# Performance work log

Measured on AMD Instinct MI355X. Metric: run time of the kernel, lower is better.

Reference implementation:

```python
import jax, jax.numpy as jnp
import numpy as np


def _dwconv3x3(x, w, b):
    # depthwise 3x3, stride 1, padding 1 (groups == channels)
    y = jax.lax.conv_general_dilated(
        x, w, window_strides=(1, 1), padding=((1, 1), (1, 1)),
        dimension_numbers=('NCHW', 'OIHW', 'NCHW'),
        feature_group_count=x.shape[1])
    return y + b[None, :, None, None]


def _maxpool(x, f):
    # adaptive_max_pool2d to (h//f, w//f) with h,w divisible by f == stride-f max pool
    return jax.lax.reduce_window(x, -jnp.inf, jax.lax.max,
                                 (1, 1, f, f), (1, 1, f, f), 'VALID')


def _up_nearest(x, f):
    return jnp.repeat(jnp.repeat(x, f, axis=2), f, axis=3)


def setup_inputs() -> dict:
    key = jax.random.key(0)
    ks = jax.random.split(key, 10)
    B, C, H, W = 4, 32, 128, 128
    x = jax.random.normal(ks[0], (B, C, H, W), dtype=jnp.float32)
    mk = lambda k, shape, s: jax.random.normal(k, shape, dtype=jnp.float32) * s
    return {
        'x': x,
        'w0': mk(ks[1], (C, 1, 3, 3), 0.3), 'b0': mk(ks[2], (C,), 0.05),
        'w1': mk(ks[3], (C, 1, 3, 3), 0.3), 'b1': mk(ks[4], (C,), 0.05),
        'w2': mk(ks[5], (C, 1, 3, 3), 0.3), 'b2': mk(ks[6], (C,), 0.05),
        'wa': mk(ks[7], (C, C, 1, 1), 0.2), 'ba': mk(ks[8], (C,), 0.05),
    }


def reference(x, w0, b0, w1, b1, w2, b2, wa, ba):
    b, c, h, w = x.shape
    # multi-scale depthwise feature refinement
    s0 = _dwconv3x3(x, w0, b0)                               # level 0: full res
    s1 = _up_nearest(_dwconv3x3(_maxpool(x, 2), w1, b1), 2)  # level 1: /2
    s2 = _up_nearest(_dwconv3x3(_maxpool(x, 4), w2, b2), 4)  # level 2: /4
    # Channel_mixing8: q=s0, k=s1, v=s2; per-pixel CxC outer product
    to_nc = lambda t: t.transpose(0, 2, 3, 1).reshape(-1, c)  # (N, C), N=b*h*w
    q, k, v = to_nc(s0), to_nc(s1), to_nc(s2)
    kv = v[:, :, None] * k[:, None, :]        # (N, C, C) = v_embed @ k_embed^T
    attn = jax.nn.softmax(kv, axis=1)         # softmax over dim=1 (v axis)
    qkv = jnp.einsum('nij,nj->ni', attn, q)   # matvec with q
    out = qkv.reshape(b, h, w, c).transpose(0, 3, 1, 2)
    # aggr: 1x1 conv; drop_path=0 -> identity
    out = jnp.einsum('bchw,oc->bohw', out, wa[:, :, 0, 0]) + ba[None, :, None, None]
    return jax.nn.gelu(out, approximate=False) * x
```

## Files before the change

kernel.cpp:

```cpp
#include <hip/hip_runtime.h>
#include <math.h>

#define BB 4
#define CC 32
#define HH 128
#define WW 128

__global__ __launch_bounds__(256) void pool_kernel(const float* __restrict__ x,
                                                   float* __restrict__ p1,
                                                   float* __restrict__ p2) {
  int idx = blockIdx.x * 256 + threadIdx.x;
  int j  = idx & 31;
  int i  = (idx >> 5) & 31;
  int bc = idx >> 10;
  const float* xp = x + ((size_t)bc * HH + 4 * i) * WW + 4 * j;
  float4 r0 = *(const float4*)(xp);
  float4 r1 = *(const float4*)(xp + WW);
  float4 r2 = *(const float4*)(xp + 2 * WW);
  float4 r3 = *(const float4*)(xp + 3 * WW);
  float m00 = fmaxf(fmaxf(r0.x, r1.x), fmaxf(r0.y, r1.y));
  float m01 = fmaxf(fmaxf(r0.z, r1.z), fmaxf(r0.w, r1.w));
  float m10 = fmaxf(fmaxf(r2.x, r3.x), fmaxf(r2.y, r3.y));
  float m11 = fmaxf(fmaxf(r2.z, r3.z), fmaxf(r2.w, r3.w));
  float* pp = p1 + ((size_t)bc * 64 + 2 * i) * 64 + 2 * j;
  pp[0]  = m00; pp[1]  = m01;
  pp[64] = m10; pp[65] = m11;
  p2[(size_t)bc * 1024 + i * 32 + j] = fmaxf(fmaxf(m00, m01), fmaxf(m10, m11));
}

template <int HS, int WS, int HSH, int WSH>
__global__ __launch_bounds__(256) void dwconv_kernel(const float* __restrict__ in,
                                                     const float* __restrict__ wt,
                                                     const float* __restrict__ bias,
                                                     float* __restrict__ out) {
  int idx = blockIdx.x * 256 + threadIdx.x;
  int w_ = idx & (WS - 1);
  int h_ = (idx >> WSH) & (HS - 1);
  int bc = idx >> (WSH + HSH);
  int c  = bc & (CC - 1);
  const float* ip = in + (size_t)bc * (HS * WS);
  float wv[9];
#pragma unroll
  for (int t = 0; t < 9; ++t) wv[t] = wt[c * 9 + t];
  float acc = bias[c];
#pragma unroll
  for (int dh = 0; dh < 3; ++dh) {
    int hh = h_ + dh - 1;
    if ((unsigned)hh >= (unsigned)HS) continue;
#pragma unroll
    for (int dw = 0; dw < 3; ++dw) {
      int ww = w_ + dw - 1;
      if ((unsigned)ww >= (unsigned)WS) continue;
      acc = fmaf(wv[dh * 3 + dw], ip[hh * WS + ww], acc);
    }
  }
  out[idx] = acc;
}

__global__ __launch_bounds__(256) void mix_kernel(const float* __restrict__ s0,
                                                  const float* __restrict__ c1,
                                                  const float* __restrict__ c2,
                                                  const float* __restrict__ x,
                                                  const float* __restrict__ wa,
                                                  const float* __restrict__ ba,
                                                  float* __restrict__ out) {
  int n  = blockIdx.x * 256 + threadIdx.x;
  int w_ = n & (WW - 1);
  int h_ = (n >> 7) & (HH - 1);
  int b  = n >> 14;
  size_t base0 = ((size_t)(b * CC) * HH + h_) * WW + w_;
  size_t base1 = ((size_t)(b * CC) * 64 + (h_ >> 1)) * 64 + (w_ >> 1);
  size_t base2 = ((size_t)(b * CC) * 32 + (h_ >> 2)) * 32 + (w_ >> 2);

  float v[CC], e[CC], qkv[CC];
#pragma unroll
  for (int i = 0; i < CC; ++i) {
    v[i]   = c2[base2 + i * 1024];
    qkv[i] = 0.f;
  }
  float vmax = v[0], vmin = v[0];
#pragma unroll
  for (int i = 1; i < CC; ++i) {
    vmax = fmaxf(vmax, v[i]);
    vmin = fminf(vmin, v[i]);
  }

  const float L2E = 1.4426950408889634f;
  float kj = c1[base1];
  float qj = s0[base0];
  for (int j = 0; j < CC; ++j) {
    float kjn = 0.f, qjn = 0.f;
    if (j + 1 < CC) {
      kjn = c1[base1 + (size_t)(j + 1) * 4096];
      qjn = s0[base0 + (size_t)(j + 1) * 16384];
    }
    float m  = (kj >= 0.f) ? kj * vmax : kj * vmin;
    float kl = kj * L2E;
    float nm = -m * L2E;
    float d0 = 0.f, d1 = 0.f, d2 = 0.f, d3 = 0.f;
#pragma unroll
    for (int i = 0; i < CC; i += 4) {
      e[i]     = __builtin_amdgcn_exp2f(fmaf(v[i],     kl, nm)); d0 += e[i];
      e[i + 1] = __builtin_amdgcn_exp2f(fmaf(v[i + 1], kl, nm)); d1 += e[i + 1];
      e[i + 2] = __builtin_amdgcn_exp2f(fmaf(v[i + 2], kl, nm)); d2 += e[i + 2];
      e[i + 3] = __builtin_amdgcn_exp2f(fmaf(v[i + 3], kl, nm)); d3 += e[i + 3];
    }
    float denom = (d0 + d1) + (d2 + d3);
    float scale = __fdividef(qj, denom);
#pragma unroll
    for (int i = 0; i < CC; ++i) qkv[i] = fmaf(scale, e[i], qkv[i]);
    kj = kjn;
    qj = qjn;
  }

  for (int o = 0; o < CC; ++o) {
    float y = ba[o];
#pragma unroll
    for (int c2i = 0; c2i < CC; ++c2i) y = fmaf(wa[o * CC + c2i], qkv[c2i], y);
    float g = 0.5f * y * (1.f + erff(y * 0.70710678118654752f));
    size_t oi = base0 + (size_t)o * (HH * WW);
    out[oi] = g * x[oi];
  }
}

extern "C" void kernel_launch(void* const* d_in, const int* in_sizes, int n_in,
                              void* d_out, int out_size, void* d_ws, size_t ws_size,
                              hipStream_t stream) {
  const float* x  = (const float*)d_in[0];
  const float* w0 = (const float*)d_in[1];
  const float* b0 = (const float*)d_in[2];
  const float* w1 = (const float*)d_in[3];
  const float* b1 = (const float*)d_in[4];
  const float* w2 = (const float*)d_in[5];
  const float* b2 = (const float*)d_in[6];
  const float* wa = (const float*)d_in[7];
  const float* ba = (const float*)d_in[8];
  float* out = (float*)d_out;

  float* ws = (float*)d_ws;
  float* s0 = ws;
  float* p1 = s0 + 2097152;
  float* c1 = p1 + 524288;
  float* p2 = c1 + 524288;
  float* c2 = p2 + 131072;

  pool_kernel<<<512, 256, 0, stream>>>(x, p1, p2);
  dwconv_kernel<128, 128, 7, 7><<<8192, 256, 0, stream>>>(x, w0, b0, s0);
  dwconv_kernel<64, 64, 6, 6><<<2048, 256, 0, stream>>>(p1, w1, b1, c1);
  dwconv_kernel<32, 32, 5, 5><<<512, 256, 0, stream>>>(p2, w2, b2, c2);
  mix_kernel<<<256, 256, 0, stream>>>(s0, c1, c2, x, wa, ba, out);
}
```

Baseline: 128.4 us.

## Share softmax exponentials across pixels with equal k,v and split mixing kernel

The fused per-pixel mixing kernel is split into an attention kernel and an epilogue kernel. The attention kernel exploits that k is constant over 2x2 blocks and v over 4x4 blocks. Each exp/softmax column is computed once per distinct (k,v) pair in shared memory and reused by the four pixels that share it, which cuts exp work about fourfold. Results are written to a global qkv buffer that the epilogue reads for the 1x1 conv, GELU and multiply by x. This trades extra global traffic and a launch for less transcendental work and better parallelism (2048 blocks instead of 256).

```diff
diff --git a/kernel.cpp b/kernel.cpp
--- a/kernel.cpp
+++ b/kernel.cpp
@@ -57,69 +57,130 @@
   out[idx] = acc;
 }
 
-__global__ __launch_bounds__(256) void mix_kernel(const float* __restrict__ s0,
-                                                  const float* __restrict__ c1,
-                                                  const float* __restrict__ c2,
+__global__ __launch_bounds__(256) void attn_kernel(const float* __restrict__ s0,
+                                                   const float* __restrict__ c1,
+                                                   const float* __restrict__ c2,
+                                                   float* __restrict__ qkv_g) {
+  int bid = blockIdx.x;
+  int tw = bid & 7;
+  int th = (bid >> 3) & 63;
+  int b  = bid >> 9;
+  int t  = threadIdx.x;
+
+  __shared__ __align__(16) float vsh[8 * 36];
+  __shared__ __align__(16) float Ebuf[8 * 1036];
+  __shared__ float scaleT[32 * 33];
+
+  {
+    int eb = t >> 5, i = t & 31;
+    int h4 = th >> 1;
+    int w4 = tw * 4 + (eb >> 1);
+    vsh[eb * 36 + i] = c2[((size_t)(b * CC + i) * 32 + h4) * 32 + w4];
+  }
+  __syncthreads();
+
+  {
+    int eb = t >> 5, j = t & 31;
+    float kj = c1[((size_t)(b * CC + j) * 64 + th) * 64 + (tw * 8 + eb)];
+    float vv[32];
+    const float4* v4 = (const float4*)(vsh + eb * 36);
+#pragma unroll
+    for (int iq = 0; iq < 8; ++iq) {
+      float4 q_ = v4[iq];
+      vv[4 * iq] = q_.x; vv[4 * iq + 1] = q_.y; vv[4 * iq + 2] = q_.z; vv[4 * iq + 3] = q_.w;
+    }
+    float vmax = vv[0], vmin = vv[0];
+#pragma unroll
+    for (int i = 1; i < CC; ++i) {
+      vmax = fmaxf(vmax, vv[i]);
+      vmin = fminf(vmin, vv[i]);
+    }
+    const float L2E = 1.4426950408889634f;
+    float m  = (kj >= 0.f) ? kj * vmax : kj * vmin;
+    float kl = kj * L2E;
+    float nm = -m * L2E;
+    float d0 = 0.f, d1 = 0.f, d2 = 0.f, d3 = 0.f;
+    float* Ecol = Ebuf + eb * 1036 + j;
+#pragma unroll
+    for (int i = 0; i < CC; i += 4) {
+      float e0 = __builtin_amdgcn_exp2f(fmaf(vv[i],     kl, nm)); Ecol[i * 32]       = e0; d0 += e0;
+      float e1 = __builtin_amdgcn_exp2f(fmaf(vv[i + 1], kl, nm)); Ecol[(i + 1) * 32] = e1; d1 += e1;
+      float e2 = __builtin_amdgcn_exp2f(fmaf(vv[i + 2], kl, nm)); Ecol[(i + 2) * 32] = e2; d2 += e2;
+      float e3 = __builtin_amdgcn_exp2f(fmaf(vv[i + 3], kl, nm)); Ecol[(i + 3) * 32] = e3; d3 += e3;
+    }
+    float rd = __fdividef(1.f, (d0 + d1) + (d2 + d3));
+    int h0 = th * 2, w0 = tw * 16;
+    size_t qb = ((size_t)(b * CC + j) * HH + h0) * WW + w0 + eb * 2;
+#pragma unroll
+    for (int px = 0; px < 4; ++px) {
+      int hh = px >> 1, wwb = px & 1;
+      float q = s0[qb + hh * WW + wwb];
+      scaleT[j * 33 + (hh * 16 + eb * 2 + wwb)] = q * rd;
+    }
+  }
+  __syncthreads();
+
+  {
+    int p = t & 31, ic = t >> 5;
+    int eb = (p & 15) >> 1;
+    const float* Er = Ebuf + eb * 1036 + ic * 128;
+    float a0 = 0.f, a1 = 0.f, a2 = 0.f, a3 = 0.f;
+#pragma unroll
+    for (int jq = 0; jq < 8; ++jq) {
+      float4 e0 = *(const float4*)(Er + jq * 4);
+      float4 e1 = *(const float4*)(Er + 32 + jq * 4);
+      float4 e2 = *(const float4*)(Er + 64 + jq * 4);
+      float4 e3 = *(const float4*)(Er + 96 + jq * 4);
+      float s0v = scaleT[(jq * 4)     * 33 + p];
+      float s1v = scaleT[(jq * 4 + 1) * 33 + p];
+      float s2v = scaleT[(jq * 4 + 2) * 33 + p];
+      float s3v = scaleT[(jq * 4 + 3) * 33 + p];
+      a0 = fmaf(e0.x, s0v, fmaf(e0.y, s1v, fmaf(e0.z, s2v, fmaf(e0.w, s3v, a0))));
+      a1 = fmaf(e1.x, s0v, fmaf(e1.y, s1v, fmaf(e1.z, s2v, fmaf(e1.w, s3v, a1))));
+      a2 = fmaf(e2.x, s0v, fmaf(e2.y, s1v, fmaf(e2.z, s2v, fmaf(e2.w, s3v, a2))));
+      a3 = fmaf(e3.x, s0v, fmaf(e3.y, s1v, fmaf(e3.z, s2v, fmaf(e3.w, s3v, a3))));
+    }
+    int hh = p >> 4, ww = p & 15;
+    int n = ((b * HH + th * 2 + hh) * WW + tw * 16 + ww);
+    int i0 = ic * 4;
+    qkv_g[(size_t)(i0 + 0) * 65536 + n] = a0;
+    qkv_g[(size_t)(i0 + 1) * 65536 + n] = a1;
+    qkv_g[(size_t)(i0 + 2) * 65536 + n] = a2;
+    qkv_g[(size_t)(i0 + 3) * 65536 + n] = a3;
+  }
+}
+
+__global__ __launch_bounds__(256) void epi_kernel(const float* __restrict__ qkv_g,
                                                   const float* __restrict__ x,
                                                   const float* __restrict__ wa,
                                                   const float* __restrict__ ba,
                                                   float* __restrict__ out) {
-  int n  = blockIdx.x * 256 + threadIdx.x;
-  int w_ = n & (WW - 1);
-  int h_ = (n >> 7) & (HH - 1);
-  int b  = n >> 14;
-  size_t base0 = ((size_t)(b * CC) * HH + h_) * WW + w_;
-  size_t base1 = ((size_t)(b * CC) * 64 + (h_ >> 1)) * 64 + (w_ >> 1);
-  size_t base2 = ((size_t)(b * CC) * 32 + (h_ >> 2)) * 32 + (w_ >> 2);
-
-  float v[CC], e[CC], qkv[CC];
-#pragma unroll
-  for (int i = 0; i < CC; ++i) {
-    v[i]   = c2[base2 + i * 1024];
-    qkv[i] = 0.f;
-  }
-  float vmax = v[0], vmin = v[0];
-#pragma unroll
-  for (int i = 1; i < CC; ++i) {
-    vmax = fmaxf(vmax, v[i]);
-    vmin = fminf(vmin, v[i]);
-  }
-
-  const float L2E = 1.4426950408889634f;
-  float kj = c1[base1];
-  float qj = s0[base0];
-  for (int j = 0; j < CC; ++j) {
-    float kjn = 0.f, qjn = 0.f;
-    if (j + 1 < CC) {
-      kjn = c1[base1 + (size_t)(j + 1) * 4096];
-      qjn = s0[base0 + (size_t)(j + 1) * 16384];
-    }
-    float m  = (kj >= 0.f) ? kj * vmax : kj * vmin;
-    float kl = kj * L2E;
-    float nm = -m * L2E;
-    float d0 = 0.f, d1 = 0.f, d2 = 0.f, d3 = 0.f;
-#pragma unroll
-    for (int i = 0; i < CC; i += 4) {
-      e[i]     = __builtin_amdgcn_exp2f(fmaf(v[i],     kl, nm)); d0 += e[i];
-      e[i + 1] = __builtin_amdgcn_exp2f(fmaf(v[i + 1], kl, nm)); d1 += e[i + 1];
-      e[i + 2] = __builtin_amdgcn_exp2f(fmaf(v[i + 2], kl, nm)); d2 += e[i + 2];
-      e[i + 3] = __builtin_amdgcn_exp2f(fmaf(v[i + 3], kl, nm)); d3 += e[i + 3];
-    }
-    float denom = (d0 + d1) + (d2 + d3);
-    float scale = __fdividef(qj, denom);
-#pragma unroll
-    for (int i = 0; i < CC; ++i) qkv[i] = fmaf(scale, e[i], qkv[i]);
-    kj = kjn;
-    qj = qjn;
-  }
-
-  for (int o = 0; o < CC; ++o) {
-    float y = ba[o];
-#pragma unroll
-    for (int c2i = 0; c2i < CC; ++c2i) y = fmaf(wa[o * CC + c2i], qkv[c2i], y);
-    float g = 0.5f * y * (1.f + erff(y * 0.70710678118654752f));
-    size_t oi = base0 + (size_t)o * (HH * WW);
-    out[oi] = g * x[oi];
+  int n = blockIdx.x * 256 + threadIdx.x;
+  float qkv[CC];
+#pragma unroll
+  for (int i = 0; i < CC; ++i) qkv[i] = qkv_g[(size_t)i * 65536 + n];
+  int bo = (n >> 14) * CC;
+  int hw = n & 16383;
+  for (int ob = 0; ob < CC; ob += 4) {
+    float y0 = ba[ob], y1 = ba[ob + 1], y2 = ba[ob + 2], y3 = ba[ob + 3];
+#pragma unroll
+    for (int i = 0; i < CC; ++i) {
+      float qv = qkv[i];
+      y0 = fmaf(wa[(ob)     * CC + i], qv, y0);
+      y1 = fmaf(wa[(ob + 1) * CC + i], qv, y1);
+      y2 = fmaf(wa[(ob + 2) * CC + i], qv, y2);
+      y3 = fmaf(wa[(ob + 3) * CC + i], qv, y3);
+    }
+    const float RS2 = 0.70710678118654752f;
+    float g0 = 0.5f * y0 * (1.f + erff(y0 * RS2));
+    float g1 = 0.5f * y1 * (1.f + erff(y1 * RS2));
+    float g2 = 0.5f * y2 * (1.f + erff(y2 * RS2));
+    float g3 = 0.5f * y3 * (1.f + erff(y3 * RS2));
+    size_t oi0 = (size_t)(bo + ob) * 16384 + hw;
+    out[oi0]           = g0 * x[oi0];
+    out[oi0 + 16384]   = g1 * x[oi0 + 16384];
+    out[oi0 + 32768]   = g2 * x[oi0 + 32768];
+    out[oi0 + 49152]   = g3 * x[oi0 + 49152];
   }
 }
 
@@ -143,10 +204,12 @@
   float* c1 = p1 + 524288;
   float* p2 = c1 + 524288;
   float* c2 = p2 + 131072;
+  float* qkv_g = c2 + 131072;
 
   pool_kernel<<<512, 256, 0, stream>>>(x, p1, p2);
   dwconv_kernel<128, 128, 7, 7><<<8192, 256, 0, stream>>>(x, w0, b0, s0);
   dwconv_kernel<64, 64, 6, 6><<<2048, 256, 0, stream>>>(p1, w1, b1, c1);
   dwconv_kernel<32, 32, 5, 5><<<512, 256, 0, stream>>>(p2, w2, b2, c2);
-  mix_kernel<<<256, 256, 0, stream>>>(s0, c1, c2, x, wa, ba, out);
-}
+  attn_kernel<<<2048, 256, 0, stream>>>(s0, c1, c2, qkv_g);
+  epi_kernel<<<256, 256, 0, stream>>>(qkv_g, x, wa, ba, out);
+}
```

Result: slower. 133.8 us (+4.2%).
